# Kernel tuning notes

Hardware: AMD Instinct MI355X
Metric: run time of the kernel (lower is better)

The kernel has to match this reference:

```python
import jax, jax.numpy as jnp
import numpy as np

H, KV, D = 12, 4, 128  # n_head, n_kv_head, head_dim
VE_GATE_CH = 12

def _rmsnorm(x):
    eps = jnp.finfo(x.dtype).eps  # matches torch F.rms_norm default eps
    return x * jax.lax.rsqrt(jnp.mean(x * x, axis=-1, keepdims=True) + eps)

def _rope(x, cos, sin):
    d = x.shape[-1] // 2
    x1, x2 = x[..., :d], x[..., d:]
    return jnp.concatenate([x1 * cos + x2 * sin, -x1 * sin + x2 * cos], axis=-1)

def setup_inputs() -> dict:
    key = jax.random.key(0)
    ks = jax.random.split(key, 9)
    B, T, C = 2, 2048, 1536
    x = jax.random.normal(ks[0], (B, T, C), jnp.float32)
    ve = jax.random.normal(ks[1], (B, T, KV * D), jnp.float32)
    ang = jax.random.uniform(ks[2], (1, T, 1, D // 2), jnp.float32) * (2.0 * np.pi)
    cos, sin = jnp.cos(ang), jnp.sin(ang)
    Wq = jax.random.normal(ks[3], (H * D, C), jnp.float32) * 0.02
    Wk = jax.random.normal(ks[4], (KV * D, C), jnp.float32) * 0.02
    Wv = jax.random.normal(ks[5], (KV * D, C), jnp.float32) * 0.02
    Wproj = jax.random.normal(ks[6], (C, C), jnp.float32) * 0.02
    Wg = jax.random.normal(ks[7], (KV, VE_GATE_CH), jnp.float32) * 0.02
    return dict(x=x, ve=ve, cos=cos, sin=sin, Wq=Wq, Wk=Wk, Wv=Wv, Wproj=Wproj, Wg=Wg, window=1024)

def reference(x, ve, cos, sin, Wq, Wk, Wv, Wproj, Wg, window):
    B, T, C = x.shape
    q = (x @ Wq.T).reshape(B, T, H, D)
    k = (x @ Wk.T).reshape(B, T, KV, D)
    v = (x @ Wv.T).reshape(B, T, KV, D)
    # value-embedding gate: 3*sigmoid(Linear(x[..., :12])) per kv head
    gate = 3.0 * jax.nn.sigmoid(x[..., :VE_GATE_CH] @ Wg.T)  # [B,T,KV]
    v = v + gate[..., None] * ve.reshape(B, T, KV, D)
    q = _rmsnorm(_rope(q, cos, sin)) * 1.2
    k = _rmsnorm(_rope(k, cos, sin)) * 1.2
    rep = H // KV  # GQA group size
    qh = q.transpose(0, 2, 1, 3).reshape(B, KV, rep, T, D)
    kh = k.transpose(0, 2, 1, 3)  # [B,KV,T,D]
    vh = v.transpose(0, 2, 1, 3)
    scores = jnp.einsum('bgrtd,bgsd->bgrts', qh, kh) / np.sqrt(D)
    row = jnp.arange(T)[:, None]
    col = jnp.arange(T)[None, :]
    if window < 0 or window >= T:
        mask = col <= row  # pure causal
    else:
        mask = (col <= row) & (row - col <= window)  # causal sliding window
    scores = jnp.where(mask, scores, -jnp.inf)
    att = jax.nn.softmax(scores, axis=-1)
    y = jnp.einsum('bgrts,bgsd->bgrtd', att, vh)
    y = y.reshape(B, H, T, D).transpose(0, 2, 1, 3).reshape(B, T, H * D)
    return y @ Wproj.T
```

## Files before the change

### kernel.cpp

```cpp
#include <hip/hip_runtime.h>
#include <hip/hip_bf16.h>
#include <math.h>

#define B_  2
#define T_  2048
#define C_  1536
#define H_  12
#define KV_ 4
#define D_  128
#define M_  (B_*T_)
#define REP_ (H_/KV_)
#define NQKV_ 2560
#define KK_  1536
#define NKT_ 24

typedef __bf16 bf16x8 __attribute__((ext_vector_type(8)));
typedef float  f32x4  __attribute__((ext_vector_type(4)));
typedef unsigned u32x4 __attribute__((ext_vector_type(4)));

union BCast { u32x4 u; bf16x8 b; };

__device__ inline bf16x8 ldb8(const ushort* p) {
    BCast c; c.u = *reinterpret_cast<const u32x4*>(p); return c.b;
}

__device__ inline ushort f2bf(float f) {
    union { float f; unsigned u; } v; v.f = f;
    unsigned u = v.u;
    return (ushort)((u + 0x7FFF + ((u >> 16) & 1)) >> 16);
}

__device__ inline float bf2f(ushort u) {
    union { unsigned u; float f; } v; v.u = (unsigned)u << 16;
    return v.f;
}

__device__ inline void async_copy16(const ushort* g, ushort* l) {
    __builtin_amdgcn_global_load_lds(
        (const __attribute__((address_space(1))) unsigned*)g,
        (__attribute__((address_space(3))) unsigned*)l, 16, 0, 0);
}

__device__ __host__ inline int dperm(int d) {
    return (d < 32) ? d : (d < 64 ? d + 32 : (d < 96 ? d - 32 : d));
}

__device__ __forceinline__ void phase_barrier() {
    __builtin_amdgcn_sched_barrier(0);
    __builtin_amdgcn_s_barrier();
    __builtin_amdgcn_sched_barrier(0);
}
__device__ __forceinline__ void lgkm0_fence() {
    __builtin_amdgcn_s_waitcnt(0xC07F);
    __builtin_amdgcn_sched_barrier(0);
}
__device__ __forceinline__ bf16x8 frag_ld(const ushort* half, int row, int kbyte) {
    const int byt = (row << 7) + (kbyte ^ ((row & 7) << 4));
    return ldb8((const ushort*)((const char*)half + byt));
}
#define MFMA16(va, vb, d) d = __builtin_amdgcn_mfma_f32_16x16x32_bf16(va, vb, d, 0, 0, 0)

template<int EPI>
__global__ __launch_bounds__(512) void gemm256(const ushort* __restrict__ A,
                                               const ushort* __restrict__ Bm,
                                               ushort* __restrict__ Qp,
                                               ushort* __restrict__ Kp,
                                               ushort* __restrict__ vbuf,
                                               float* __restrict__ Cf,
                                               const float* __restrict__ cosb,
                                               const float* __restrict__ sinb) {
    __shared__ ushort lds[2][2][2][8192];
    const int tid  = threadIdx.x;
    const int wave = tid >> 6, lane = tid & 63;
    const int m16 = lane & 15, quad = lane >> 4;
    const int WM = wave >> 2, WN = wave & 3;
    const int bm = blockIdx.y << 8, bn = blockIdx.x << 8;
    const int brow = (WN & 1) << 6;

    const int r = tid >> 3;
    const int slot8 = ((tid & 7) ^ (r & 7)) << 3;
    const ushort* Ag = A  + (size_t)(bm + r) * KK_ + slot8;
    const ushort* Bg = Bm + (size_t)(bn + r) * KK_ + slot8;
    const size_t row64 = (size_t)64 * KK_;
    const size_t hskip = (size_t)128 * KK_;

    ushort* lbase = &lds[0][0][0][0];
    const int wlds = wave << 9;

    auto stage2 = [&](const ushort* Gp, int buf, int op, int kc) {
        ushort* l0 = lbase + (((buf*2 + op)*2 + 0) << 13) + wlds;
        ushort* l1 = lbase + (((buf*2 + op)*2 + 1) << 13) + wlds;
        const ushort* g = Gp + kc;
        async_copy16(g,                 l0);
        async_copy16(g + row64,         l0 + 4096);
        async_copy16(g + hskip,         l1);
        async_copy16(g + hskip + row64, l1 + 4096);
    };

    f32x4 acc[8][4];
    #pragma unroll
    for (int i = 0; i < 8; i++)
        #pragma unroll
        for (int j = 0; j < 4; j++) acc[i][j] = (f32x4){0.f, 0.f, 0.f, 0.f};

    stage2(Bg, 0, 1, 0);  stage2(Ag, 0, 0, 0);
    stage2(Bg, 1, 1, 64); stage2(Ag, 1, 0, 64);
    __builtin_amdgcn_s_waitcnt(0x0F78);
    phase_barrier();

    #pragma unroll 1
    for (int kt = 0; kt < NKT_; kt++) {
        const int buf = kt & 1;
        const ushort* Ah = lbase + (((buf*2 + 0)*2 + WM)        << 13);
        const ushort* Bh = lbase + (((buf*2 + 1)*2 + (WN >> 1)) << 13);
        const int kc2 = (kt + 2) << 6;
        const bool stg = (kt < NKT_ - 2);

        bf16x8 a[8], b0[4], b1[4];
        #pragma unroll
        for (int mf = 0; mf < 4; mf++) {
            a[mf*2+0] = frag_ld(Ah, mf*16 + m16, quad*16);
            a[mf*2+1] = frag_ld(Ah, mf*16 + m16, 64 + quad*16);
        }
        #pragma unroll
        for (int nf = 0; nf < 2; nf++) {
            b0[nf*2+0] = frag_ld(Bh, brow + nf*16 + m16, quad*16);
            b0[nf*2+1] = frag_ld(Bh, brow + nf*16 + m16, 64 + quad*16);
        }
        phase_barrier();
        lgkm0_fence();
        __builtin_amdgcn_s_setprio(1);
        #pragma unroll
        for (int mf = 0; mf < 4; mf++)
            #pragma unroll
            for (int nf = 0; nf < 2; nf++) {
                MFMA16(a[mf*2+0], b0[nf*2+0], acc[mf][nf]);
                MFMA16(a[mf*2+1], b0[nf*2+1], acc[mf][nf]);
            }
        __builtin_amdgcn_s_setprio(0);
        phase_barrier();
        #pragma unroll
        for (int nf = 0; nf < 2; nf++) {
            b1[nf*2+0] = frag_ld(Bh, brow + 32 + nf*16 + m16, quad*16);
            b1[nf*2+1] = frag_ld(Bh, brow + 32 + nf*16 + m16, 64 + quad*16);
        }
        phase_barrier();
        lgkm0_fence();
        __builtin_amdgcn_s_setprio(1);
        #pragma unroll
        for (int mf = 0; mf < 4; mf++)
            #pragma unroll
            for (int nf = 0; nf < 2; nf++) {
                MFMA16(a[mf*2+0], b1[nf*2+0], acc[mf][2+nf]);
                MFMA16(a[mf*2+1], b1[nf*2+1], acc[mf][2+nf]);
            }
        __builtin_amdgcn_s_setprio(0);
        phase_barrier();
        #pragma unroll
        for (int mf = 0; mf < 4; mf++) {
            a[mf*2+0] = frag_ld(Ah, 64 + mf*16 + m16, quad*16);
            a[mf*2+1] = frag_ld(Ah, 64 + mf*16 + m16, 64 + quad*16);
        }
        if (stg) stage2(Bg, buf, 1, kc2);
        phase_barrier();
        lgkm0_fence();
        __builtin_amdgcn_s_setprio(1);
        #pragma unroll
        for (int mf = 0; mf < 4; mf++)
            #pragma unroll
            for (int nf = 0; nf < 2; nf++) {
                MFMA16(a[mf*2+0], b1[nf*2+0], acc[4+mf][2+nf]);
                MFMA16(a[mf*2+1], b1[nf*2+1], acc[4+mf][2+nf]);
            }
        __builtin_amdgcn_s_setprio(0);
        phase_barrier();
        if (stg) stage2(Ag, buf, 0, kc2);
        phase_barrier();
        __builtin_amdgcn_s_setprio(1);
        #pragma unroll
        for (int mf = 0; mf < 4; mf++)
            #pragma unroll
            for (int nf = 0; nf < 2; nf++) {
                MFMA16(a[mf*2+0], b0[nf*2+0], acc[4+mf][nf]);
                MFMA16(a[mf*2+1], b0[nf*2+1], acc[4+mf][nf]);
            }
        __builtin_amdgcn_s_setprio(0);
        if (stg)                 __builtin_amdgcn_s_waitcnt(0x0F78);
        else if (kt == NKT_ - 2) __builtin_amdgcn_s_waitcnt(0x0F70);
        phase_barrier();
    }

    if constexpr (EPI == 0) {
        if (bn >= 2048) {
            const int cb = bn - 2048 + WN*64;
            #pragma unroll
            for (int m = 0; m < 8; m++) {
                const int rl = WM*128 + (m>>2)*64 + (m&3)*16 + quad*4;
                #pragma unroll
                for (int reg = 0; reg < 4; reg++) {
                    ushort* vr = vbuf + (size_t)(bm + rl + reg) * 512 + cb + m16;
                    #pragma unroll
                    for (int j = 0; j < 4; j++)
                        vr[(j>>1)*32 + (j&1)*16] = f2bf(acc[m][j][reg]);
                }
            }
        } else {
            float* ssqS = (float*)lbase;
            #pragma unroll
            for (int m = 0; m < 8; m++) {
                #pragma unroll
                for (int reg = 0; reg < 4; reg++) {
                    float v = acc[m][0][reg]*acc[m][0][reg] + acc[m][1][reg]*acc[m][1][reg]
                            + acc[m][2][reg]*acc[m][2][reg] + acc[m][3][reg]*acc[m][3][reg];
                    v += __shfl_xor(v, 1); v += __shfl_xor(v, 2);
                    v += __shfl_xor(v, 4); v += __shfl_xor(v, 8);
                    if (m16 == 0) {
                        const int rl = WM*128 + (m>>2)*64 + (m&3)*16 + quad*4 + reg;
                        ssqS[rl*4 + WN] = v;
                    }
                }
            }
            __syncthreads();

            const bool isq = (bn < 1536);
            const float osc = isq ? (1.2f * 1.2f * 0.08838834764831845f) : 1.0f;
            const int hh = (isq ? (bn >> 7) : ((bn - 1536) >> 7)) + (WN >> 1);
            const int nh  = isq ? H_ : KV_;
            ushort* outp  = isq ? Qp : Kp;

            #pragma unroll
            for (int m = 0; m < 8; m++) {
                #pragma unroll
                for (int reg = 0; reg < 4; reg++) {
                    const int rl = WM*128 + (m>>2)*64 + (m&3)*16 + quad*4 + reg;
                    const int row = bm + rl;
                    const float tot = ssqS[rl*4 + (WN & ~1)] + ssqS[rl*4 + (WN | 1)];
                    const float sc = rsqrtf(tot * (1.0f/128.0f) + 1.1920928955078125e-07f) * osc;
                    const int b = row >> 11, t = row & (T_ - 1);
                    ushort* orow = outp + ((size_t)(b * nh + hh) * T_ + t) * D_;
                    #pragma unroll
                    for (int nf = 0; nf < 2; nf++) {
                        const int ipair = (WN & 1) * 32 + nf*16 + m16;
                        const float c = cosb[t*64 + ipair], s = sinb[t*64 + ipair];
                        const float x1 = acc[m][nf][reg], x2 = acc[m][2+nf][reg];
                        const int oc = (WN & 1) * 64 + nf*16 + m16;
                        orow[oc]      = f2bf((x1*c + x2*s) * sc);
                        orow[oc + 32] = f2bf((x2*c - x1*s) * sc);
                    }
                }
            }
        }
    } else {
        #pragma unroll
        for (int m = 0; m < 8; m++) {
            const int rl = WM*128 + (m>>2)*64 + (m&3)*16 + quad*4;
            #pragma unroll
            for (int reg = 0; reg < 4; reg++) {
                float* cr = Cf + (size_t)(bm + rl + reg) * C_ + bn + WN*64 + m16;
                #pragma unroll
                for (int j = 0; j < 4; j++)
                    cr[(j>>1)*32 + (j&1)*16] = acc[m][j][reg];
            }
        }
    }
}

#define SEG0 1572864
#define SEG1 2162688
#define SEG2 2359296
#define SEG3 2555904
#define SEG4 3145728
#define ROW4 384
__global__ __launch_bounds__(256) void cast_all(const float* __restrict__ x,
                                                const float* __restrict__ Wq,
                                                const float* __restrict__ Wk,
                                                const float* __restrict__ Wv,
                                                const float* __restrict__ Wp,
                                                ushort* __restrict__ xb,
                                                ushort* __restrict__ Wqkvb,
                                                ushort* __restrict__ Wpb) {
    const int i = blockIdx.x * 256 + threadIdx.x;
    float4 v; size_t dst4; ushort* dstp;
    if (i < SEG0) {
        v = ((const float4*)x)[i]; dstp = xb; dst4 = i;
    } else if (i < SEG1) {
        const int j = i - SEG0;
        const int r = j / ROW4, c4 = j - r * ROW4;
        const int d = r & 127, hh = r >> 7;
        v = ((const float4*)Wq)[j]; dstp = Wqkvb;
        dst4 = (size_t)(hh * 128 + dperm(d)) * ROW4 + c4;
    } else if (i < SEG2) {
        const int j = i - SEG1;
        const int r = j / ROW4, c4 = j - r * ROW4;
        const int d = r & 127, g = r >> 7;
        v = ((const float4*)Wk)[j]; dstp = Wqkvb;
        dst4 = (size_t)(1536 + g * 128 + dperm(d)) * ROW4 + c4;
    } else if (i < SEG3) {
        const int j = i - SEG2;
        v = ((const float4*)Wv)[j]; dstp = Wqkvb;
        dst4 = (size_t)2048 * ROW4 + j;
    } else {
        const int j = i - SEG3;
        v = ((const float4*)Wp)[j]; dstp = Wpb; dst4 = j;
    }
    ((ushort4*)dstp)[dst4] = make_ushort4(f2bf(v.x), f2bf(v.y), f2bf(v.z), f2bf(v.w));
}

__global__ __launch_bounds__(256) void gate_vt(const ushort* __restrict__ vbuf,
                                               const float* __restrict__ x,
                                               const float* __restrict__ ve,
                                               const float* __restrict__ Wg,
                                               ushort* __restrict__ Vt) {
    const int t0 = blockIdx.x * 64, g = blockIdx.y, b = blockIdx.z;
    __shared__ float gateS[64];
    __shared__ ushort tile[128][66];
    const int tid = threadIdx.x;
    if (tid < 64) {
        const float* xr = x + (size_t)(b * T_ + t0 + tid) * C_;
        float acc = 0.f;
        #pragma unroll
        for (int c = 0; c < 12; c++) acc += xr[c] * Wg[g * 12 + c];
        gateS[tid] = 3.0f / (1.0f + __expf(-acc));
    }
    __syncthreads();
    #pragma unroll
    for (int i = 0; i < 32; i++) {
        int idx = i * 256 + tid;
        int r = idx >> 7;
        int d = idx & 127;
        size_t offv = (size_t)(b * T_ + t0 + r) * 512 + g * D_ + d;
        tile[d][r] = f2bf(bf2f(vbuf[offv]) + gateS[r] * ve[offv]);
    }
    __syncthreads();
    ushort* ob = Vt + ((size_t)(b * KV_ + g) * D_) * T_ + t0;
    #pragma unroll
    for (int i = 0; i < 32; i++) {
        int idx = i * 256 + tid;
        int d = idx >> 6;
        int c = idx & 63;
        ob[(size_t)d * T_ + c] = tile[d][c];
    }
}

__global__ __launch_bounds__(256, 3) void attn_mfma(const ushort* __restrict__ Qp,
                                                    const ushort* __restrict__ Kp,
                                                    const ushort* __restrict__ Vt,
                                                    ushort* __restrict__ Y,
                                                    const int* __restrict__ wptr) {
    const int t0 = blockIdx.x * 64;
    const int h  = blockIdx.y, b = blockIdx.z;
    const int g  = h / REP_;
    const int tid  = threadIdx.x;
    const int wave = tid >> 6, lane = tid & 63;
    const int m16 = lane & 15, quad = lane >> 4;

    __shared__ ushort Ks[4 * 32 * 32];
    __shared__ ushort Vs[128 * 32];
    __shared__ ushort Pl[4][16 * 40];

    const int w = *wptr;
    const bool windowed = (w >= 0 && w < T_);
    const unsigned wu = windowed ? (unsigned)w : 0x7FFFFFFFu;
    int s_lo = 0;
    if (windowed) { s_lo = t0 - w; if (s_lo < 0) s_lo = 0; }
    const int s_hi = t0 + 63;
    const int ss0 = s_lo & ~31;
    const int tw = t0 + wave * 16;

    const ushort* qrow = Qp + ((size_t)(b * H_ + h) * T_ + tw + m16) * D_ + quad * 8;
    bf16x8 qa[4];
    #pragma unroll
    for (int kc = 0; kc < 4; kc++) qa[kc] = ldb8(qrow + kc * 32);

    const ushort* kbase = Kp + (size_t)(b * KV_ + g) * T_ * D_;
    const ushort* vbase = Vt + (size_t)(b * KV_ + g) * D_ * T_;

    const int c0 = wave, c1 = wave + 4;
    const ushort* kg0 = kbase + (size_t)((c0 & 1) * 16 + (lane >> 2)) * D_ + (c0 >> 1) * 32 + (lane & 3) * 8;
    const ushort* kg1 = kbase + (size_t)((c1 & 1) * 16 + (lane >> 2)) * D_ + (c1 >> 1) * 32 + (lane & 3) * 8;
    ushort* kl0 = Ks + c0 * 512;
    ushort* kl1 = Ks + c1 * 512;
    const ushort* vg0 = vbase + (size_t)(c0 * 16 + (lane >> 2)) * T_ + (lane & 3) * 8;
    const ushort* vg1 = vbase + (size_t)(c1 * 16 + (lane >> 2)) * T_ + (lane & 3) * 8;
    ushort* vl0 = Vs + c0 * 512;
    ushort* vl1 = Vs + c1 * 512;

    f32x4 o[8];
    #pragma unroll
    for (int dt = 0; dt < 8; dt++) o[dt] = (f32x4){0.f, 0.f, 0.f, 0.f};
    f32x4 lacc = (f32x4){0.f, 0.f, 0.f, 0.f};
    BCast onesc; onesc.u = (u32x4){0x3F803F80u, 0x3F803F80u, 0x3F803F80u, 0x3F803F80u};
    const bf16x8 ones = onesc.b;
    ushort* pw = &Pl[wave][0];

    for (int ss = ss0; ss <= s_hi; ss += 32) {
        const size_t koff = (size_t)ss * D_;
        async_copy16(kg0 + koff, kl0);
        async_copy16(kg1 + koff, kl1);
        async_copy16(vg0 + ss,   vl0);
        async_copy16(vg1 + ss,   vl1);
        __syncthreads();

        f32x4 s0 = (f32x4){0.f,0.f,0.f,0.f};
        f32x4 s1 = (f32x4){0.f,0.f,0.f,0.f};
        #pragma unroll
        for (int kc = 0; kc < 4; kc++) {
            bf16x8 kf0 = ldb8(Ks + kc * 1024 + m16 * 32 + quad * 8);
            bf16x8 kf1 = ldb8(Ks + kc * 1024 + (16 + m16) * 32 + quad * 8);
            s0 = __builtin_amdgcn_mfma_f32_16x16x32_bf16(qa[kc], kf0, s0, 0, 0, 0);
            s1 = __builtin_amdgcn_mfma_f32_16x16x32_bf16(qa[kc], kf1, s1, 0, 0, 0);
        }

        const int sA = ss + m16, sB = ss + 16 + m16;
        #pragma unroll
        for (int reg = 0; reg < 4; reg++) {
            const int t = tw + quad * 4 + reg;
            const float pa = ((unsigned)(t - sA) <= wu) ? __expf(s0[reg]) : 0.f;
            const float pb = ((unsigned)(t - sB) <= wu) ? __expf(s1[reg]) : 0.f;
            pw[(quad * 4 + reg) * 40 + m16]      = f2bf(pa);
            pw[(quad * 4 + reg) * 40 + 16 + m16] = f2bf(pb);
        }

        __builtin_amdgcn_s_waitcnt(0xc07f);
        bf16x8 pfrag = ldb8(pw + m16 * 40 + quad * 8);

        #pragma unroll
        for (int dt = 0; dt < 8; dt++) {
            bf16x8 vf = ldb8(Vs + (dt * 16 + m16) * 32 + quad * 8);
            o[dt] = __builtin_amdgcn_mfma_f32_16x16x32_bf16(pfrag, vf, o[dt], 0, 0, 0);
        }
        lacc = __builtin_amdgcn_mfma_f32_16x16x32_bf16(pfrag, ones, lacc, 0, 0, 0);
        __syncthreads();
    }

    float inv[4];
    #pragma unroll
    for (int reg = 0; reg < 4; reg++) inv[reg] = 1.0f / lacc[reg];
    ushort* yb = Y + ((size_t)(b * T_ + tw + quad * 4) * H_ + h) * D_ + m16;
    #pragma unroll
    for (int reg = 0; reg < 4; reg++)
        #pragma unroll
        for (int dt = 0; dt < 8; dt++)
            yb[(size_t)reg * H_ * D_ + dt * 16] = f2bf(o[dt][reg] * inv[reg]);
}

extern "C" void kernel_launch(void* const* d_in, const int* in_sizes, int n_in,
                              void* d_out, int out_size, void* d_ws, size_t ws_size,
                              hipStream_t stream) {
    const float* x     = (const float*)d_in[0];
    const float* ve    = (const float*)d_in[1];
    const float* cosb  = (const float*)d_in[2];
    const float* sinb  = (const float*)d_in[3];
    const float* Wq    = (const float*)d_in[4];
    const float* Wk    = (const float*)d_in[5];
    const float* Wv    = (const float*)d_in[6];
    const float* Wproj = (const float*)d_in[7];
    const float* Wg    = (const float*)d_in[8];
    const int*   wptr  = (const int*)d_in[9];
    float* out = (float*)d_out;

    ushort* xb    = (ushort*)d_ws;
    ushort* vbuf  = xb    + (size_t)M_ * C_;
    ushort* Qp    = vbuf  + (size_t)M_ * 512;
    ushort* Kp    = Qp    + (size_t)M_ * C_;
    ushort* Vt    = Kp    + (size_t)M_ * 512;
    ushort* yb16  = Vt    + (size_t)M_ * 512;
    ushort* Wqkvb = yb16  + (size_t)M_ * C_;
    ushort* Wpb   = Wqkvb + (size_t)NQKV_ * C_;

    cast_all<<<SEG4 / 256, 256, 0, stream>>>(x, Wq, Wk, Wv, Wproj, xb, Wqkvb, Wpb);

    gemm256<0><<<dim3(NQKV_ / 256, M_ / 256), 512, 0, stream>>>(
        xb, Wqkvb, Qp, Kp, vbuf, nullptr, cosb, sinb);

    gate_vt<<<dim3(T_ / 64, KV_, B_), 256, 0, stream>>>(vbuf, x, ve, Wg, Vt);

    attn_mfma<<<dim3(T_ / 64, H_, B_), 256, 0, stream>>>(Qp, Kp, Vt, yb16, wptr);

    gemm256<1><<<dim3(C_ / 256, M_ / 256), 512, 0, stream>>>(
        yb16, Wpb, nullptr, nullptr, nullptr, out, nullptr, nullptr);
}
```

Before: 268.7 us.

## Software-pipeline LDS fragment reads in GEMM and remap blocks across XCDs

```diff
diff --git a/kernel.cpp b/kernel.cpp
--- a/kernel.cpp
+++ b/kernel.cpp
@@ -45,20 +45,36 @@
     return (d < 32) ? d : (d < 64 ? d + 32 : (d < 96 ? d - 32 : d));
 }
 
-__device__ __forceinline__ void phase_barrier() {
-    __builtin_amdgcn_sched_barrier(0);
-    __builtin_amdgcn_s_barrier();
-    __builtin_amdgcn_sched_barrier(0);
-}
 __device__ __forceinline__ void lgkm0_fence() {
     __builtin_amdgcn_s_waitcnt(0xC07F);
     __builtin_amdgcn_sched_barrier(0);
 }
-__device__ __forceinline__ bf16x8 frag_ld(const ushort* half, int row, int kbyte) {
-    const int byt = (row << 7) + (kbyte ^ ((row & 7) << 4));
-    return ldb8((const ushort*)((const char*)half + byt));
-}
+
 #define MFMA16(va, vb, d) d = __builtin_amdgcn_mfma_f32_16x16x32_bf16(va, vb, d, 0, 0, 0)
+
+#define CLUSTER(AARR, BARR, MB, NB)                                        \
+    __builtin_amdgcn_s_setprio(1);                                         \
+    _Pragma("unroll")                                                      \
+    for (int mf = 0; mf < 4; mf++)                                         \
+        _Pragma("unroll")                                                  \
+        for (int nf = 0; nf < 2; nf++) {                                   \
+            MFMA16(AARR[mf*2+0], BARR[nf*2+0], acc[(MB)+mf][(NB)+nf]);     \
+            MFMA16(AARR[mf*2+1], BARR[nf*2+1], acc[(MB)+mf][(NB)+nf]);     \
+        }                                                                  \
+    __builtin_amdgcn_s_setprio(0);
+
+#define RD_AL(bo_) { _Pragma("unroll") for (int mf = 0; mf < 4; mf++) {    \
+        aL[mf*2+0] = ldb8(aB0 + (bo_) + mf*1024);                          \
+        aL[mf*2+1] = ldb8(aB1 + (bo_) + mf*1024); } }
+#define RD_AH(bo_) { _Pragma("unroll") for (int mf = 0; mf < 4; mf++) {    \
+        aH[mf*2+0] = ldb8(aB0 + (bo_) + 4096 + mf*1024);                   \
+        aH[mf*2+1] = ldb8(aB1 + (bo_) + 4096 + mf*1024); } }
+#define RD_B0(bo_) { _Pragma("unroll") for (int nf = 0; nf < 2; nf++) {    \
+        b0[nf*2+0] = ldb8(bB0 + (bo_) + nf*1024);                          \
+        b0[nf*2+1] = ldb8(bB1 + (bo_) + nf*1024); } }
+#define RD_B1(bo_) { _Pragma("unroll") for (int nf = 0; nf < 2; nf++) {    \
+        b1[nf*2+0] = ldb8(bB0 + (bo_) + 2048 + nf*1024);                   \
+        b1[nf*2+1] = ldb8(bB1 + (bo_) + 2048 + nf*1024); } }
 
 template<int EPI>
 __global__ __launch_bounds__(512) void gemm256(const ushort* __restrict__ A,
@@ -74,8 +90,14 @@
     const int wave = tid >> 6, lane = tid & 63;
     const int m16 = lane & 15, quad = lane >> 4;
     const int WM = wave >> 2, WN = wave & 3;
-    const int bm = blockIdx.y << 8, bn = blockIdx.x << 8;
     const int brow = (WN & 1) << 6;
+
+    const int nwg  = gridDim.x * gridDim.y;
+    const int orig = blockIdx.y * gridDim.x + blockIdx.x;
+    const int vid  = (orig & 7) * (nwg >> 3) + (orig >> 3);
+    const int bxT  = vid >> 4;
+    const int byT  = vid & 15;
+    const int bm = byT << 8, bn = bxT << 8;
 
     const int r = tid >> 3;
     const int slot8 = ((tid & 7) ^ (r & 7)) << 3;
@@ -84,111 +106,82 @@
     const size_t row64 = (size_t)64 * KK_;
     const size_t hskip = (size_t)128 * KK_;
 
-    ushort* lbase = &lds[0][0][0][0];
-    const int wlds = wave << 9;
-
     auto stage2 = [&](const ushort* Gp, int buf, int op, int kc) {
-        ushort* l0 = lbase + (((buf*2 + op)*2 + 0) << 13) + wlds;
-        ushort* l1 = lbase + (((buf*2 + op)*2 + 1) << 13) + wlds;
+        ushort* base = &lds[0][0][0][0] + op * 32768 + buf * 16384 + wave * 512;
         const ushort* g = Gp + kc;
-        async_copy16(g,                 l0);
-        async_copy16(g + row64,         l0 + 4096);
-        async_copy16(g + hskip,         l1);
-        async_copy16(g + hskip + row64, l1 + 4096);
+        async_copy16(g,                 base);
+        async_copy16(g + row64,         base + 4096);
+        async_copy16(g + hskip,         base + 8192);
+        async_copy16(g + hskip + row64, base + 8192 + 4096);
     };
 
+    const int swzu = (m16 & 7) << 3;
+    const int k0u  = (quad * 8) ^ swzu;
+    const int k1u  = (32 + quad * 8) ^ swzu;
+    const ushort* ldsu = &lds[0][0][0][0];
+    const ushort* aB0 = ldsu + (WM ? 8192 : 0) + (m16 << 6) + k0u;
+    const ushort* aB1 = ldsu + (WM ? 8192 : 0) + (m16 << 6) + k1u;
+    const ushort* bB0 = ldsu + 32768 + ((WN >> 1) ? 8192 : 0) + ((brow + m16) << 6) + k0u;
+    const ushort* bB1 = ldsu + 32768 + ((WN >> 1) ? 8192 : 0) + ((brow + m16) << 6) + k1u;
+
     f32x4 acc[8][4];
     #pragma unroll
     for (int i = 0; i < 8; i++)
         #pragma unroll
         for (int j = 0; j < 4; j++) acc[i][j] = (f32x4){0.f, 0.f, 0.f, 0.f};
+
+    bf16x8 aL[8], aH[8], b0[4], b1[4];
 
     stage2(Bg, 0, 1, 0);  stage2(Ag, 0, 0, 0);
     stage2(Bg, 1, 1, 64); stage2(Ag, 1, 0, 64);
     __builtin_amdgcn_s_waitcnt(0x0F78);
-    phase_barrier();
+    __builtin_amdgcn_sched_barrier(0);
+    __builtin_amdgcn_s_barrier();
+    __builtin_amdgcn_sched_barrier(0);
+    RD_AL(0); RD_B0(0);
 
     #pragma unroll 1
-    for (int kt = 0; kt < NKT_; kt++) {
-        const int buf = kt & 1;
-        const ushort* Ah = lbase + (((buf*2 + 0)*2 + WM)        << 13);
-        const ushort* Bh = lbase + (((buf*2 + 1)*2 + (WN >> 1)) << 13);
+    for (int kt = 0; kt < NKT_ - 1; kt++) {
+        const int bo  = (kt & 1) ? 16384 : 0;
+        const int boN = 16384 - bo;
+        const bool stg = (kt < NKT_ - 2);
         const int kc2 = (kt + 2) << 6;
-        const bool stg = (kt < NKT_ - 2);
-
-        bf16x8 a[8], b0[4], b1[4];
-        #pragma unroll
-        for (int mf = 0; mf < 4; mf++) {
-            a[mf*2+0] = frag_ld(Ah, mf*16 + m16, quad*16);
-            a[mf*2+1] = frag_ld(Ah, mf*16 + m16, 64 + quad*16);
-        }
-        #pragma unroll
-        for (int nf = 0; nf < 2; nf++) {
-            b0[nf*2+0] = frag_ld(Bh, brow + nf*16 + m16, quad*16);
-            b0[nf*2+1] = frag_ld(Bh, brow + nf*16 + m16, 64 + quad*16);
-        }
-        phase_barrier();
-        lgkm0_fence();
-        __builtin_amdgcn_s_setprio(1);
-        #pragma unroll
-        for (int mf = 0; mf < 4; mf++)
-            #pragma unroll
-            for (int nf = 0; nf < 2; nf++) {
-                MFMA16(a[mf*2+0], b0[nf*2+0], acc[mf][nf]);
-                MFMA16(a[mf*2+1], b0[nf*2+1], acc[mf][nf]);
-            }
-        __builtin_amdgcn_s_setprio(0);
-        phase_barrier();
-        #pragma unroll
-        for (int nf = 0; nf < 2; nf++) {
-            b1[nf*2+0] = frag_ld(Bh, brow + 32 + nf*16 + m16, quad*16);
-            b1[nf*2+1] = frag_ld(Bh, brow + 32 + nf*16 + m16, 64 + quad*16);
-        }
-        phase_barrier();
-        lgkm0_fence();
-        __builtin_amdgcn_s_setprio(1);
-        #pragma unroll
-        for (int mf = 0; mf < 4; mf++)
-            #pragma unroll
-            for (int nf = 0; nf < 2; nf++) {
-                MFMA16(a[mf*2+0], b1[nf*2+0], acc[mf][2+nf]);
-                MFMA16(a[mf*2+1], b1[nf*2+1], acc[mf][2+nf]);
-            }
-        __builtin_amdgcn_s_setprio(0);
-        phase_barrier();
-        #pragma unroll
-        for (int mf = 0; mf < 4; mf++) {
-            a[mf*2+0] = frag_ld(Ah, 64 + mf*16 + m16, quad*16);
-            a[mf*2+1] = frag_ld(Ah, 64 + mf*16 + m16, 64 + quad*16);
-        }
-        if (stg) stage2(Bg, buf, 1, kc2);
-        phase_barrier();
-        lgkm0_fence();
-        __builtin_amdgcn_s_setprio(1);
-        #pragma unroll
-        for (int mf = 0; mf < 4; mf++)
-            #pragma unroll
-            for (int nf = 0; nf < 2; nf++) {
-                MFMA16(a[mf*2+0], b1[nf*2+0], acc[4+mf][2+nf]);
-                MFMA16(a[mf*2+1], b1[nf*2+1], acc[4+mf][2+nf]);
-            }
-        __builtin_amdgcn_s_setprio(0);
-        phase_barrier();
-        if (stg) stage2(Ag, buf, 0, kc2);
-        phase_barrier();
-        __builtin_amdgcn_s_setprio(1);
-        #pragma unroll
-        for (int mf = 0; mf < 4; mf++)
-            #pragma unroll
-            for (int nf = 0; nf < 2; nf++) {
-                MFMA16(a[mf*2+0], b0[nf*2+0], acc[4+mf][nf]);
-                MFMA16(a[mf*2+1], b0[nf*2+1], acc[4+mf][nf]);
-            }
-        __builtin_amdgcn_s_setprio(0);
-        if (stg)                 __builtin_amdgcn_s_waitcnt(0x0F78);
-        else if (kt == NKT_ - 2) __builtin_amdgcn_s_waitcnt(0x0F70);
-        phase_barrier();
-    }
+        lgkm0_fence();
+        RD_B1(bo);
+        CLUSTER(aL, b0, 0, 0);
+        lgkm0_fence();
+        RD_AH(bo);
+        CLUSTER(aL, b1, 0, 2);
+        lgkm0_fence();
+        __builtin_amdgcn_s_barrier();
+        __builtin_amdgcn_sched_barrier(0);
+        if (stg) {
+            stage2(Bg, kt & 1, 1, kc2);
+            stage2(Ag, kt & 1, 0, kc2);
+            __builtin_amdgcn_s_waitcnt(0x0F78);
+        } else {
+            __builtin_amdgcn_s_waitcnt(0x0F70);
+        }
+        __builtin_amdgcn_sched_barrier(0);
+        __builtin_amdgcn_s_barrier();
+        __builtin_amdgcn_sched_barrier(0);
+        CLUSTER(aH, b0, 4, 0);
+        RD_AL(boN); RD_B0(boN);
+        CLUSTER(aH, b1, 4, 2);
+    }
+    {
+        const int bo = ((NKT_ - 1) & 1) ? 16384 : 0;
+        lgkm0_fence();
+        RD_B1(bo);
+        CLUSTER(aL, b0, 0, 0);
+        lgkm0_fence();
+        RD_AH(bo);
+        CLUSTER(aL, b1, 0, 2);
+        lgkm0_fence();
+        CLUSTER(aH, b0, 4, 0);
+        CLUSTER(aH, b1, 4, 2);
+    }
+    __syncthreads();
 
     if constexpr (EPI == 0) {
         if (bn >= 2048) {
@@ -205,7 +198,7 @@
                 }
             }
         } else {
-            float* ssqS = (float*)lbase;
+            float* ssqS = (float*)&lds[0][0][0][0];
             #pragma unroll
             for (int m = 0; m < 8; m++) {
                 #pragma unroll
```

Measured after the change: 262.8 us. 2.2% less time.
